# Performance work log

Hardware: AMD Instinct MI355X
Metric: run time of the kernel (lower is better)

Reference implementation:

```python
import jax, jax.numpy as jnp
import numpy as np
import math

H = 12  # num_heads
LOGIT_SCALE_MAX = math.log(1.0 / 0.01)  # ~4.60517


def setup_inputs() -> dict:
    key = jax.random.key(0)
    ks = jax.random.split(key, 4)
    L, N, C = 1024, 8, 768
    scale = (C // H) ** -0.5
    return {
        "x": jax.random.normal(ks[0], (L, N, C), jnp.float32),
        "in_proj_weight": jax.random.normal(ks[1], (3 * C, C), jnp.float32) * scale,
        "in_proj_bias": jnp.zeros((3 * C,), jnp.float32),
        "logit_scale": jnp.full((H, 1, 1), jnp.log(10.0), jnp.float32),
        "head_scale": jnp.ones((H, 1, 1), jnp.float32),
        "out_w": jax.random.normal(ks[2], (C, C), jnp.float32) * scale,
        "out_b": jnp.zeros((C,), jnp.float32),
    }


def _normalize(t, eps=1e-12):
    # torch F.normalize: x / max(||x||, eps)
    n = jnp.linalg.norm(t, axis=-1, keepdims=True)
    return t / jnp.maximum(n, eps)


def reference(x, in_proj_weight, in_proj_bias, logit_scale, head_scale, out_w, out_b):
    L, N, C = x.shape
    D = C // H
    qkv = x @ in_proj_weight.T + in_proj_bias  # (L, N, 3C)
    q, k, v = jnp.split(qkv, 3, axis=-1)

    def to_heads(t):  # (L, N, C) -> (N, H, L, D); matches view(L, N*H, D).transpose(0,1)
        return t.reshape(L, N, H, D).transpose(1, 2, 0, 3)

    q, k, v = to_heads(q), to_heads(k), to_heads(v)
    # scaled-cosine attention: cosine sim * clamped-exp learnable logit scale
    attn = jnp.einsum('nhld,nhmd->nhlm', _normalize(q), _normalize(k))  # (N,H,L,L)
    ls = jnp.exp(jnp.minimum(logit_scale, LOGIT_SCALE_MAX))  # (H,1,1)
    attn = attn * ls[None]
    attn = jax.nn.softmax(attn, axis=-1)
    o = jnp.einsum('nhlm,nhmd->nhld', attn, v)  # (N,H,L,D)
    o = o * head_scale[None]  # per-head scale
    o = o.transpose(2, 0, 1, 3).reshape(L, N, C)  # back to (L, N, C)
    return o @ out_w.T + out_b
```

## Files before the change

### kernel.cpp

```cpp
#include <hip/hip_runtime.h>
#include <stdint.h>
#include <math.h>

typedef unsigned short u16;
typedef _Float16 f16;
typedef __attribute__((ext_vector_type(4))) float f32x4;
typedef __attribute__((ext_vector_type(8))) f16 h8;
typedef __attribute__((ext_vector_type(4))) f16 h4;
typedef __attribute__((ext_vector_type(2))) f16 h2;
typedef __attribute__((ext_vector_type(2))) __fp16 fp16x2;
typedef __attribute__((ext_vector_type(2))) unsigned int u32x2;
typedef __attribute__((ext_vector_type(4))) unsigned int u32x4;
typedef __attribute__((ext_vector_type(4))) unsigned short u16x4;
typedef __attribute__((ext_vector_type(8))) unsigned short u16x8;

typedef const __attribute__((address_space(1))) u16 gas_u16;
typedef __attribute__((address_space(3))) u16 las_u16;

#define MFMA32(a,b,c) __builtin_amdgcn_mfma_f32_16x16x32_f16((a),(b),(c),0,0,0)
#define MFMA16(a,b,c) __builtin_amdgcn_mfma_f32_16x16x16f16((a),(b),(c),0,0,0)

__device__ __forceinline__ float h2f(u16 h){ f16 x; __builtin_memcpy(&x,&h,2); return (float)x; }
__device__ __forceinline__ u16 f2h(float f){ f16 x = (f16)f; u16 u; __builtin_memcpy(&u,&x,2); return u; }

__device__ __forceinline__ float fast_exp2(float x){
#if __has_builtin(__builtin_amdgcn_exp2f)
  return __builtin_amdgcn_exp2f(x);
#else
  return exp2f(x);
#endif
}

__device__ __forceinline__ h2 pkrtz(float a, float b){
  fp16x2 t = __builtin_amdgcn_cvt_pkrtz(a, b);
  h2 r; __builtin_memcpy(&r, &t, 4);
  return r;
}

#define NA4 1572864
#define NB4 442368
#define NC4 147456
__global__ __launch_bounds__(256) void cvt3_kernel(
    const float* __restrict__ a, u16* __restrict__ da,
    const float* __restrict__ b, u16* __restrict__ db,
    const float* __restrict__ c, u16* __restrict__ dc)
{
  int i = blockIdx.x*256 + threadIdx.x;
  const float* s; u16* d; int off;
  if (i < NA4)            { s = a; d = da; off = i; }
  else if (i < NA4+NB4)   { s = b; d = db; off = i - NA4; }
  else if (i < NA4+NB4+NC4){ s = c; d = dc; off = i - NA4 - NB4; }
  else return;
  f32x4 v = ((const f32x4*)s)[off];
  u16x4 o;
  o[0]=f2h(v[0]); o[1]=f2h(v[1]); o[2]=f2h(v[2]); o[3]=f2h(v[3]);
  ((u16x4*)d)[off] = o;
}

__global__ __launch_bounds__(256) void gemm_kernel(
    const u16* __restrict__ A, const u16* __restrict__ B, const float* __restrict__ bias,
    int mode, u16* __restrict__ qh, u16* __restrict__ kh, u16* __restrict__ vtp,
    float* __restrict__ outp, const float* __restrict__ lsb)
{
  __shared__ u16 lA[2][128*64];
  __shared__ u16 lB[2][128*64];
  const int tid = threadIdx.x;
  const int lane = tid & 63;
  const int w = tid >> 6, wr = w >> 1, wc = w & 1;
  const int lo = lane & 15, hi = lane >> 4;

  const int bx = blockIdx.x, by = blockIdx.y;

  f32x4 zero = {0.f,0.f,0.f,0.f};
  f32x4 acc[4][4];
#pragma unroll
  for (int a=0;a<4;a++)
#pragma unroll
    for (int b=0;b<4;b++) acc[a][b] = zero;
  const u16* Ag = A + (size_t)bx*128*768;
  const u16* Bg = B + (size_t)by*128*768;
  const int srow = tid >> 3;
  const int scol = (((tid & 7) ^ (srow & 7)) * 8);

#define STAGE(buf, kt) do { \
    _Pragma("unroll") \
    for (int j=0;j<4;j++) { \
      __builtin_amdgcn_global_load_lds((gas_u16*)(Ag + (size_t)(j*32+srow)*768 + (kt) + scol), (las_u16*)(&lA[buf][j*2048 + tid*8]), 16, 0, 0); \
      __builtin_amdgcn_global_load_lds((gas_u16*)(Bg + (size_t)(j*32+srow)*768 + (kt) + scol), (las_u16*)(&lB[buf][j*2048 + tid*8]), 16, 0, 0); \
    } \
  } while(0)

  STAGE(0, 0);
#pragma unroll
  for (int t = 0; t < 12; ++t) {
    const int cur = t & 1;
    if (t < 11) {
      STAGE(cur^1, (t+1)*64);
      asm volatile("s_waitcnt vmcnt(8)" ::: "memory");
    } else {
      asm volatile("s_waitcnt vmcnt(0)" ::: "memory");
    }
    __builtin_amdgcn_sched_barrier(0);
    __builtin_amdgcn_s_barrier();
#pragma unroll
    for (int kk=0;kk<2;kk++) {
      h8 af[4], bfr[4];
#pragma unroll
      for (int mf=0; mf<4; mf++) {
        int r = wr*64 + mf*16 + lo;
        af[mf]  = *(const h8*)(&lA[cur][r*64 + (((hi + 4*kk) ^ (lo & 7)) * 8)]);
      }
#pragma unroll
      for (int nf=0; nf<4; nf++) {
        int r = wc*64 + nf*16 + lo;
        bfr[nf] = *(const h8*)(&lB[cur][r*64 + (((hi + 4*kk) ^ (lo & 7)) * 8)]);
      }
#pragma unroll
      for (int mf=0; mf<4; mf++)
#pragma unroll
        for (int nf=0; nf<4; nf++)
          acc[mf][nf] = MFMA32(af[mf], bfr[nf], acc[mf][nf]);
    }
    asm volatile("s_waitcnt lgkmcnt(0)" ::: "memory");
    __builtin_amdgcn_sched_barrier(0);
    __builtin_amdgcn_s_barrier();
  }
#undef STAGE

  const int r0 = bx*128 + wr*64;
  const int j0 = by*128 + wc*64;
  if (mode == 0) {
    const int p = (j0 >= 1536) ? 2 : ((j0 >= 768) ? 1 : 0);
    float bi[4];
#pragma unroll
    for (int nf=0;nf<4;nf++) bi[nf] = bias[j0 + nf*16 + lo];
    if (p == 2) {
      u16* Tt = (wc == 0) ? (u16*)lA : (u16*)lB;
      const int cbase = wr*16;
#pragma unroll
      for (int mf=0; mf<4; mf++)
#pragma unroll
        for (int nf=0; nf<4; nf++) {
          int d = nf*16 + lo;
          int c = cbase + mf*4 + hi;
          u16x4 pk;
#pragma unroll
          for (int i=0;i<4;i++) pk[i] = f2h(acc[mf][nf][i] + bi[nf]);
          *(u16x4*)(Tt + d*128 + ((c ^ ((d & 7) << 2)) << 2)) = pk;
        }
      __syncthreads();
      const int hh0 = 2*by - 24;
#pragma unroll
      for (int kq=0; kq<8; kq++) {
        int idx = tid + kq*256;
        int nn  = idx & 7;
        int d   = (idx >> 3) & 63;
        int lh  = (idx >> 9) & 1;
        int wcc = idx >> 10;
        const u16* Ts = (wcc == 0) ? (const u16*)lA : (const u16*)lB;
        u16x8 v8;
#pragma unroll
        for (int ll=0; ll<8; ll++) {
          int rl = (lh*8 + ll)*8 + nn;
          int c  = rl >> 2;
          v8[ll] = Ts[d*128 + ((c ^ ((d & 7) << 2)) << 2) + (rl & 3)];
        }
        size_t off = (((size_t)nn*12 + hh0 + wcc)*64 + d)*1024 + (size_t)bx*16 + lh*8;
        *(u16x8*)(vtp + off) = v8;
      }
    } else {
      const int c0 = j0 - p*768;
      const int hh = c0 >> 6;
      u16* dst = (p==0) ? qh : kh;
      float qsc = 1.0f;
      if (p == 0) qsc = __expf(fminf(lsb[hh], 4.6051701859880913680f)) * 1.4426950408889634f;
#pragma unroll
      for (int mf=0; mf<4; mf++)
#pragma unroll
        for (int i=0;i<4;i++) {
          int r = r0 + mf*16 + 4*hi + i;
          int n = r & 7, l = r >> 3;
          float v[4]; float ss = 0.f;
#pragma unroll
          for (int nf=0;nf<4;nf++){ v[nf] = acc[mf][nf][i] + bi[nf]; ss += v[nf]*v[nf]; }
          ss += __shfl_xor(ss, 1);
          ss += __shfl_xor(ss, 2);
          ss += __shfl_xor(ss, 4);
          ss += __shfl_xor(ss, 8);
          float sc = qsc / fmaxf(sqrtf(ss), 1e-12f);
          size_t base = (((size_t)n*12 + hh)*1024 + l)*64;
#pragma unroll
          for (int nf=0;nf<4;nf++)
            dst[base + nf*16 + lo] = f2h(v[nf]*sc);
        }
    }
  } else {
#pragma unroll
    for (int nf=0; nf<4; nf++) {
      int j = j0 + nf*16 + lo;
      float bi = bias[j];
#pragma unroll
      for (int mf=0; mf<4; mf++)
#pragma unroll
        for (int i=0;i<4;i++) {
          int r = r0 + mf*16 + 4*hi + i;
          outp[(size_t)r*768 + j] = acc[mf][nf][i] + bi;
        }
    }
  }
}

__global__ __launch_bounds__(256, 3) void flash_kernel(
    const u16* __restrict__ qh, const u16* __restrict__ kh, const u16* __restrict__ vt,
    u16* __restrict__ obuf, const float* __restrict__ hsv, const float* __restrict__ lsp)
{
  __shared__ u16 lK[64*64];
  __shared__ u16 lVT[64*64];
  const int lin = blockIdx.y*8 + blockIdx.x;
  const int xcd = lin & 7, g = lin >> 3;
  const int nh = xcd + 8*(g >> 3);
  const int qt = g & 7;
  const int h = nh % 12, n = nh / 12;
  const u16* Qp = qh + (size_t)nh*65536;
  const u16* Kp = kh + (size_t)nh*65536;
  const u16* Vp = vt + (size_t)nh*65536;
  const int tid = threadIdx.x, lane = tid & 63, w = tid >> 6;
  const int lo = lane & 15, hi = lane >> 4;
  const int e = lo & 7;

  h8 qa0, qa1, qb0, qb1;
  {
    const u16* qrow = Qp + (size_t)(qt*128 + w*32 + lo)*64 + hi*8;
    qa0 = *(const h8*)qrow;          qa1 = *(const h8*)(qrow + 32);
    qb0 = *(const h8*)(qrow + 1024); qb1 = *(const h8*)(qrow + 1024 + 32);
  }
  const f32x4 zero = {0.f,0.f,0.f,0.f};
  f32x4 oA[4] = {zero,zero,zero,zero};
  f32x4 oB[4] = {zero,zero,zero,zero};
  f32x4 lA4 = zero, lB4 = zero;
  const h4 ones = {(f16)1.f,(f16)1.f,(f16)1.f,(f16)1.f};

  float OFF;
  {
    float b = __expf(fminf(lsp[h], 4.6051701859880913680f)) * 1.4426950408889634f;
    OFF = fmaxf(b - 15.5f, 0.f);
  }

  const int sr = tid >> 2;
  const int c4 = tid & 3;
  const int sx1 = sr & 7;
  const int sx2 = (sr & 7) << 1;

  u32x4 ka, kb, va, vb;
  ka = *(const u32x4*)(Kp + (size_t)sr*64 + c4*16);
  kb = *(const u32x4*)(Kp + (size_t)sr*64 + c4*16 + 8);
  va = *(const u32x4*)(Vp + (size_t)sr*1024 + c4*16);
  vb = *(const u32x4*)(Vp + (size_t)sr*1024 + c4*16 + 8);

  for (int t = 0; t < 16; ++t) {
    {
      u16* kr = lK + sr*64;
      *(u32x4*)(kr + (((2*c4)   ^ sx1) << 3)) = ka;
      *(u32x4*)(kr + (((2*c4+1) ^ sx1) << 3)) = kb;
      u16* vr = lVT + sr*64;
      *(u32x2*)(vr + (((( 0|c4) ^ sx2) << 2))) = (u32x2){va[0], va[1]};
      *(u32x2*)(vr + (((( 4|c4) ^ sx2) << 2))) = (u32x2){va[2], va[3]};
      *(u32x2*)(vr + (((( 8|c4) ^ sx2) << 2))) = (u32x2){vb[0], vb[1]};
      *(u32x2*)(vr + ((((12|c4) ^ sx2) << 2))) = (u32x2){vb[2], vb[3]};
    }
    asm volatile("s_waitcnt lgkmcnt(0)" ::: "memory");
    __builtin_amdgcn_sched_barrier(0);
    __builtin_amdgcn_s_barrier();
    if (t < 15) {
      ka = *(const u32x4*)(Kp + (size_t)(t+1)*4096 + (size_t)sr*64 + c4*16);
      kb = *(const u32x4*)(Kp + (size_t)(t+1)*4096 + (size_t)sr*64 + c4*16 + 8);
      va = *(const u32x4*)(Vp + (size_t)sr*1024 + (t+1)*64 + c4*16);
      vb = *(const u32x4*)(Vp + (size_t)sr*1024 + (t+1)*64 + c4*16 + 8);
    }
    f32x4 sa[4], sb[4];
#pragma unroll
    for (int kf=0; kf<4; kf++) {
      const u16* krow = lK + (kf*16 + lo)*64;
      h8 k0 = *(const h8*)(krow + (((hi  ) ^ e) << 3));
      h8 k1 = *(const h8*)(krow + (((hi+4) ^ e) << 3));
      sa[kf] = MFMA32(k1, qa1, MFMA32(k0, qa0, zero));
      sb[kf] = MFMA32(k1, qb1, MFMA32(k0, qb0, zero));
    }
    if (OFF != 0.f) {
#pragma unroll
      for (int kf=0;kf<4;kf++)
#pragma unroll
        for (int i=0;i<4;i++) { sa[kf][i] -= OFF; sb[kf][i] -= OFF; }
    }
    h4 pa[4], pb[4];
#pragma unroll
    for (int kf=0;kf<4;kf++) {
      h2 a01 = pkrtz(fast_exp2(sa[kf][0]), fast_exp2(sa[kf][1]));
      h2 a23 = pkrtz(fast_exp2(sa[kf][2]), fast_exp2(sa[kf][3]));
      pa[kf] = __builtin_shufflevector(a01, a23, 0, 1, 2, 3);
      h2 b01 = pkrtz(fast_exp2(sb[kf][0]), fast_exp2(sb[kf][1]));
      h2 b23 = pkrtz(fast_exp2(sb[kf][2]), fast_exp2(sb[kf][3]));
      pb[kf] = __builtin_shufflevector(b01, b23, 0, 1, 2, 3);
    }
#pragma unroll
    for (int kf=0;kf<4;kf++) {
      lA4 = MFMA16(ones, pa[kf], lA4);
      lB4 = MFMA16(ones, pb[kf], lB4);
    }
#pragma unroll
    for (int db=0; db<4; db++) {
      const u16* vrow = lVT + (db*16 + lo)*64;
      h8 v01 = *(const h8*)(vrow + ((((2*hi  ) ^ e) << 3)));
      h8 v23 = *(const h8*)(vrow + ((((2*hi+1) ^ e) << 3)));
      h4 f0 = __builtin_shufflevector(v01, v01, 0,1,2,3);
      h4 f1 = __builtin_shufflevector(v01, v01, 4,5,6,7);
      h4 f2 = __builtin_shufflevector(v23, v23, 0,1,2,3);
      h4 f3 = __builtin_shufflevector(v23, v23, 4,5,6,7);
      oA[db] = MFMA16(f0, pa[0], oA[db]);
      oB[db] = MFMA16(f0, pb[0], oB[db]);
      oA[db] = MFMA16(f1, pa[1], oA[db]);
      oB[db] = MFMA16(f1, pb[1], oB[db]);
      oA[db] = MFMA16(f2, pa[2], oA[db]);
      oB[db] = MFMA16(f2, pb[2], oB[db]);
      oA[db] = MFMA16(f3, pa[3], oA[db]);
      oB[db] = MFMA16(f3, pb[3], oB[db]);
    }
    asm volatile("s_waitcnt lgkmcnt(0)" ::: "memory");
    __builtin_amdgcn_sched_barrier(0);
    __builtin_amdgcn_s_barrier();
  }
  float hsc = hsv[h];
  float invA = hsc / lA4[0];
  float invB = hsc / lB4[0];
  int l0 = qt*128 + w*32 + lo;
  u16* dA = obuf + ((size_t)l0*8 + n)*768 + h*64;
  u16* dB = obuf + ((size_t)(l0+16)*8 + n)*768 + h*64;
#pragma unroll
  for (int db=0; db<4; db++) {
    u16x4 pk0, pk1;
#pragma unroll
    for (int i=0;i<4;i++) { pk0[i] = f2h(oA[db][i]*invA); pk1[i] = f2h(oB[db][i]*invB); }
    *(u16x4*)(dA + db*16 + hi*4) = pk0;
    *(u16x4*)(dB + db*16 + hi*4) = pk1;
  }
}

extern "C" void kernel_launch(void* const* d_in, const int* in_sizes, int n_in,
                              void* d_out, int out_size, void* d_ws, size_t ws_size,
                              hipStream_t stream)
{
  (void)in_sizes; (void)n_in; (void)out_size; (void)ws_size;
  const float* x  = (const float*)d_in[0];
  const float* w1 = (const float*)d_in[1];
  const float* b1 = (const float*)d_in[2];
  const float* ls = (const float*)d_in[3];
  const float* hs = (const float*)d_in[4];
  const float* w2 = (const float*)d_in[5];
  const float* b2 = (const float*)d_in[6];
  float* out = (float*)d_out;

  u16* x_bf  = (u16*)d_ws;
  u16* w1_bf = x_bf  + 6291456;
  u16* w2_bf = w1_bf + 1769472;
  u16* qh    = w2_bf + 589824;
  u16* kh    = qh    + 6291456;
  u16* vt    = kh    + 6291456;
  u16* ob    = x_bf;

  cvt3_kernel<<<8448, 256, 0, stream>>>(x, x_bf, w1, w1_bf, w2, w2_bf);
  gemm_kernel<<<dim3(64,18), 256, 0, stream>>>(x_bf, w1_bf, b1, 0, qh, kh, vt, nullptr, ls);
  flash_kernel<<<dim3(8,96), 256, 0, stream>>>(qh, kh, vt, ob, hs, ls);
  gemm_kernel<<<dim3(64,6), 256, 0, stream>>>(ob, w2_bf, b2, 1, nullptr, nullptr, nullptr, out, ls);
}
```

Before: 118.3 us.

## Double-buffer K/V shared tiles in flash kernel and stagger GEMM k-order

The flash attention kernel now keeps two LDS buffers for K and V^T. The next tile is written into the alternate buffer after the current tile's compute, which removes one barrier per iteration and lets the global-load latency overlap with compute. The QKV GEMM also alternates the kk sub-step order between waves, which is meant to spread LDS bank access. The cost is double the LDS use per block (32KB), which could lower occupancy.

```diff
diff --git a/kernel.cpp b/kernel.cpp
--- a/kernel.cpp
+++ b/kernel.cpp
@@ -103,7 +103,8 @@
     __builtin_amdgcn_sched_barrier(0);
     __builtin_amdgcn_s_barrier();
 #pragma unroll
-    for (int kk=0;kk<2;kk++) {
+    for (int s=0;s<2;s++) {
+      const int kk = s ^ (w & 1);
       h8 af[4], bfr[4];
 #pragma unroll
       for (int mf=0; mf<4; mf++) {
@@ -214,8 +215,8 @@
     const u16* __restrict__ qh, const u16* __restrict__ kh, const u16* __restrict__ vt,
     u16* __restrict__ obuf, const float* __restrict__ hsv, const float* __restrict__ lsp)
 {
-  __shared__ u16 lK[64*64];
-  __shared__ u16 lVT[64*64];
+  __shared__ u16 lK[2][64*64];
+  __shared__ u16 lVT[2][64*64];
   const int lin = blockIdx.y*8 + blockIdx.x;
   const int xcd = lin & 7, g = lin >> 3;
   const int nh = xcd + 8*(g >> 3);
@@ -257,20 +258,24 @@
   va = *(const u32x4*)(Vp + (size_t)sr*1024 + c4*16);
   vb = *(const u32x4*)(Vp + (size_t)sr*1024 + c4*16 + 8);
 
+#define STAGE_WRITE(bf) do { \
+    u16* kr = lK[bf] + sr*64; \
+    *(u32x4*)(kr + (((2*c4)   ^ sx1) << 3)) = ka; \
+    *(u32x4*)(kr + (((2*c4+1) ^ sx1) << 3)) = kb; \
+    u16* vr = lVT[bf] + sr*64; \
+    *(u32x2*)(vr + (((( 0|c4) ^ sx2) << 2))) = (u32x2){va[0], va[1]}; \
+    *(u32x2*)(vr + (((( 4|c4) ^ sx2) << 2))) = (u32x2){va[2], va[3]}; \
+    *(u32x2*)(vr + (((( 8|c4) ^ sx2) << 2))) = (u32x2){vb[0], vb[1]}; \
+    *(u32x2*)(vr + ((((12|c4) ^ sx2) << 2))) = (u32x2){vb[2], vb[3]}; \
+  } while(0)
+
+  STAGE_WRITE(0);
+  asm volatile("s_waitcnt lgkmcnt(0)" ::: "memory");
+  __builtin_amdgcn_sched_barrier(0);
+  __builtin_amdgcn_s_barrier();
+
   for (int t = 0; t < 16; ++t) {
-    {
-      u16* kr = lK + sr*64;
-      *(u32x4*)(kr + (((2*c4)   ^ sx1) << 3)) = ka;
-      *(u32x4*)(kr + (((2*c4+1) ^ sx1) << 3)) = kb;
-      u16* vr = lVT + sr*64;
-      *(u32x2*)(vr + (((( 0|c4) ^ sx2) << 2))) = (u32x2){va[0], va[1]};
-      *(u32x2*)(vr + (((( 4|c4) ^ sx2) << 2))) = (u32x2){va[2], va[3]};
-      *(u32x2*)(vr + (((( 8|c4) ^ sx2) << 2))) = (u32x2){vb[0], vb[1]};
-      *(u32x2*)(vr + ((((12|c4) ^ sx2) << 2))) = (u32x2){vb[2], vb[3]};
-    }
-    asm volatile("s_waitcnt lgkmcnt(0)" ::: "memory");
-    __builtin_amdgcn_sched_barrier(0);
-    __builtin_amdgcn_s_barrier();
+    const int cb = t & 1;
     if (t < 15) {
       ka = *(const u32x4*)(Kp + (size_t)(t+1)*4096 + (size_t)sr*64 + c4*16);
       kb = *(const u32x4*)(Kp + (size_t)(t+1)*4096 + (size_t)sr*64 + c4*16 + 8);
@@ -280,7 +285,7 @@
     f32x4 sa[4], sb[4];
 #pragma unroll
     for (int kf=0; kf<4; kf++) {
-      const u16* krow = lK + (kf*16 + lo)*64;
+      const u16* krow = lK[cb] + (kf*16 + lo)*64;
       h8 k0 = *(const h8*)(krow + (((hi  ) ^ e) << 3));
       h8 k1 = *(const h8*)(krow + (((hi+4) ^ e) << 3));
       sa[kf] = MFMA32(k1, qa1, MFMA32(k0, qa0, zero));
@@ -309,7 +314,7 @@
     }
 #pragma unroll
     for (int db=0; db<4; db++) {
-      const u16* vrow = lVT + (db*16 + lo)*64;
+      const u16* vrow = lVT[cb] + (db*16 + lo)*64;
       h8 v01 = *(const h8*)(vrow + ((((2*hi  ) ^ e) << 3)));
       h8 v23 = *(const h8*)(vrow + ((((2*hi+1) ^ e) << 3)));
       h4 f0 = __builtin_shufflevector(v01, v01, 0,1,2,3);
@@ -325,10 +330,12 @@
       oA[db] = MFMA16(f3, pa[3], oA[db]);
       oB[db] = MFMA16(f3, pb[3], oB[db]);
     }
+    if (t < 15) STAGE_WRITE(cb ^ 1);
     asm volatile("s_waitcnt lgkmcnt(0)" ::: "memory");
     __builtin_amdgcn_sched_barrier(0);
     __builtin_amdgcn_s_barrier();
   }
+#undef STAGE_WRITE
   float hsc = hsv[h];
   float invA = hsc / lA4[0];
   float invB = hsc / lB4[0];
```

Result: no change. 117.4 us (-0.7%).
